# Kernel optimization log

Hardware: AMD Instinct MI355X
Metric: run time of the kernel (lower is better)

## Reference

```python
import jax, jax.numpy as jnp
import numpy as np

D = 64        # symbol_repr_size
NCLS = 10     # n_classes; embedding row NCLS is the 'inf' token
BSZ = 1024
L = 1024      # power of 2 -> perfect segment tree, tree_len = 2*L - 1


def _rms(t):
    # matches: x / x.pow(2).mean(-1,keepdim=True).add(1e-6).sqrt().add(1e-6)
    return t / (jnp.sqrt(jnp.mean(t * t, axis=-1, keepdims=True) + 1e-6) + 1e-6)


def _gate_combine(left, right, Wr):
    # left,right: [b,n,d]; Wr: [2,d,d] (rule weight reshaped).
    # rule(vec(outer(left,right))) == einsum without materializing [b,n,d,d].
    scores = jnp.einsum('bni,kij,bnj->bnk', left, Wr, right)
    alpha = jax.nn.softmax(scores, axis=-1)                      # [b,n,2]
    return _rms(alpha[..., 0:1] * left + alpha[..., 1:2] * right)


def setup_inputs() -> dict:
    key = jax.random.key(0)
    k = jax.random.split(key, 6)
    x = jax.random.randint(k[0], (BSZ, L), 0, NCLS, dtype=jnp.int32)
    a = jax.random.randint(k[1], (BSZ,), 0, L, dtype=jnp.int32)
    b = jax.random.randint(k[2], (BSZ,), 0, L, dtype=jnp.int32)
    return {
        'x': x,
        'query_low': jnp.minimum(a, b),
        'query_high': jnp.maximum(a, b),
        'embedding': jax.random.normal(k[3], (NCLS + 1, D), jnp.float32),
        'rule_w': jax.random.normal(k[4], (2, D * D), jnp.float32) / D,
        'linear_w': jax.random.normal(k[5], (NCLS, D), jnp.float32) / 8.0,
    }


def reference(x, query_low, query_high, embedding, rule_w, linear_w):
    bsz, l = x.shape
    d = embedding.shape[1]
    Wr = rule_w.reshape(2, d, d)
    inf_tok = embedding[-1]                 # [d], the 'inf' token (row n_classes)

    h = _rms(embedding[x])                  # [b,l,d] leaf symbols

    # ---- build neural segment tree, bottom-up (vectorized per level) ----
    levels = [h]                            # levels[0] = leaves (2^depth nodes)
    cur = h
    while cur.shape[1] > 1:
        cur = _gate_combine(cur[:, 0::2], cur[:, 1::2], Wr)
        levels.append(cur)                  # parents of previous level

    # ---- range min query, bottom-up over all nodes (masked per batch) ----
    res = None
    for nodes in levels:                    # leaves first, root last
        n = nodes.shape[1]
        seg = l // n                        # segment length covered per node
        lows = jnp.arange(n, dtype=query_low.dtype) * seg
        highs = lows + (seg - 1)
        inside = (query_low[:, None] <= lows) & (query_high[:, None] >= highs)
        disjoint = (query_low[:, None] > highs) | (query_high[:, None] < lows)
        if res is None:
            # leaf: either fully inside the query range or disjoint from it
            res = jnp.where(inside[..., None], nodes, inf_tok)
        else:
            comb = _gate_combine(res[:, 0::2], res[:, 1::2], Wr)
            res = jnp.where(inside[..., None], nodes,
                            jnp.where(disjoint[..., None], inf_tok, comb))
    returns = res[:, 0]                     # root answer, [b,d]
    return returns @ linear_w.T             # logits [b, n_classes]
```

## Files before the change

kernel.cpp:

```cpp
#include <hip/hip_runtime.h>

#define NCLS 10

typedef _Float16 half8 __attribute__((ext_vector_type(8)));
typedef _Float16 h2 __attribute__((ext_vector_type(2)));
typedef __fp16 fp16x2 __attribute__((ext_vector_type(2)));
typedef float f32x4 __attribute__((ext_vector_type(4)));
typedef unsigned int u32;

#define MFMA(A, B, C) __builtin_amdgcn_mfma_f32_16x16x32_f16(A, B, C, 0, 0, 0)

union U4H8 { uint4 u; half8 h; h2 p[4]; u32 w[4]; };
union U2H4 { uint2 u; h2 p[2]; };
union HCVT { fp16x2 f; h2 h; u32 w; };

__device__ __forceinline__ int rc(int row, int c) { return (row << 3) | (c ^ (row & 7)); }
__device__ __forceinline__ h2 pk2(float a, float b) { HCVT u; u.f = __builtin_amdgcn_cvt_pkrtz(a, b); return u.h; }
__device__ __forceinline__ u32 packh2(float a, float b) { HCVT u; u.f = __builtin_amdgcn_cvt_pkrtz(a, b); return u.w; }
__device__ __forceinline__ float fdot2f(h2 a, h2 b, float c) { return __builtin_amdgcn_fdot2(a, b, c, false); }
__device__ __forceinline__ float wave_sum(float v) {
#pragma unroll
    for (int m = 1; m < 64; m <<= 1) v += __shfl_xor(v, m, 64);
    return v;
}
__device__ __forceinline__ float red4(float v) {
    v += __shfl_xor(v, 16, 64);
    v += __shfl_xor(v, 32, 64);
    return v;
}

template <int N, bool EXACT>
__device__ __forceinline__ void combine(const uint4* src, const int (&rowL)[N],
                                        const int (&rowR)[N], const half8 (&wfd)[2][4],
                                        int pl, int g, U4H8 (&q)[N][2]) {
    U4H8 La[N][2], Ra[N][2];
#pragma unroll
    for (int n = 0; n < N; ++n)
#pragma unroll
        for (int kb = 0; kb < 2; ++kb) {
            La[n][kb].u = src[rc(rowL[n], g + 4 * kb)];
            Ra[n][kb].u = src[rc(rowR[n], g + 4 * kb)];
        }
    const uint2* s2 = (const uint2*)src;
    U2H4 rv[N][4];
#pragma unroll
    for (int n = 0; n < N; ++n)
#pragma unroll
        for (int mb = 0; mb < 4; ++mb)
            rv[n][mb].u = s2[rc(rowR[n], 2 * mb + (g >> 1)) * 2 + (g & 1)];
    float sd[N], lr[N], ll[N], rr[N];
#pragma unroll
    for (int n = 0; n < N; ++n) { sd[n] = 0.f; lr[n] = 0.f; ll[n] = 0.f; rr[n] = 0.f; }
#pragma unroll
    for (int mb = 0; mb < 4; ++mb)
#pragma unroll
        for (int n = 0; n < N; ++n) {
            f32x4 t = {0.f, 0.f, 0.f, 0.f};
#pragma unroll
            for (int kb = 0; kb < 2; ++kb) t = MFMA(wfd[kb][mb], La[n][kb].h, t);
            sd[n] = fdot2f(pk2(t[0], t[1]), rv[n][mb].p[0],
                           fdot2f(pk2(t[2], t[3]), rv[n][mb].p[1], sd[n]));
        }
#pragma unroll
    for (int n = 0; n < N; ++n)
#pragma unroll
        for (int kb = 0; kb < 2; ++kb)
#pragma unroll
            for (int i = 0; i < 4; ++i) {
                h2 l2 = La[n][kb].p[i], r2 = Ra[n][kb].p[i];
                lr[n] = fdot2f(l2, r2, lr[n]);
                if (EXACT) { ll[n] = fdot2f(l2, l2, ll[n]); rr[n] = fdot2f(r2, r2, rr[n]); }
            }
#pragma unroll
    for (int n = 0; n < N; ++n) {
        sd[n] = red4(sd[n]); lr[n] = red4(lr[n]);
        if (EXACT) { ll[n] = red4(ll[n]); rr[n] = red4(rr[n]); }
    }
#pragma unroll
    for (int n = 0; n < N; ++n) {
        float u = __expf(sd[n]);
        float a0 = __builtin_amdgcn_rcpf(1.f + u), a1 = 1.f - a0;
        float ms = EXACT ? (a0 * a0 * ll[n] + 2.f * a0 * a1 * lr[n] + a1 * a1 * rr[n]) * (1.f / 64.f)
                         : a0 * a0 + a1 * a1 + a0 * a1 * lr[n] * (2.f / 64.f);
        float sc = __builtin_amdgcn_rcpf(__builtin_amdgcn_sqrtf(ms + 1e-6f) + 1e-6f);
        h2 c0 = pk2(a0 * sc, a0 * sc), c1 = pk2(a1 * sc, a1 * sc);
#pragma unroll
        for (int kb = 0; kb < 2; ++kb)
#pragma unroll
            for (int i = 0; i < 4; ++i)
                q[n][kb].p[i] = c0 * La[n][kb].p[i] + c1 * Ra[n][kb].p[i];
    }
}


__device__ __forceinline__ void load_wfd(const uint4* ws4, half8 (&wfd)[2][4], int lane) {
#pragma unroll
    for (int fm = 0; fm < 8; ++fm) {
        U4H8 t;
        t.u = ws4[fm * 64 + lane];
        wfd[fm >> 2][fm & 3] = t.h;
    }
}

__global__ void setup_kernel(const float* __restrict__ emb,
                             const float* __restrict__ rule_w, uint4* __restrict__ ws4) {
    int tid = threadIdx.x;
    int idx = blockIdx.x * 256 + tid;
    {
        int e2 = idx & 3, lane = (idx >> 2) & 63, fm = idx >> 8;
        int kb = fm >> 2, mb = fm & 3, pl = lane & 15, g = lane >> 4;
        int i0 = 32 * kb + 8 * g + 2 * e2, j = 16 * mb + pl;
        float d0 = rule_w[4096 + i0 * 64 + j] - rule_w[i0 * 64 + j];
        float d1 = rule_w[4096 + (i0 + 1) * 64 + j] - rule_w[(i0 + 1) * 64 + j];
        ((u32*)ws4)[idx] = packh2(d0, d1);
    }
    if (blockIdx.x == 0 && tid < 64) {
        int lane = tid;
        u32* eg = (u32*)(ws4 + 512);
        for (int r = 0; r < 11; ++r) {
            float e = emb[r * 64 + lane];
            float ms = wave_sum(e * e) * (1.f / 64.f);
            float v = e * __builtin_amdgcn_rcpf(__builtin_amdgcn_sqrtf(ms + 1e-6f) + 1e-6f);
            u32 w = packh2(v, __shfl_xor(v, 1, 64));
            if ((lane & 1) == 0) eg[r * 32 + (lane >> 1)] = w;
        }
        float e = emb[640 + lane];
        u32 w = packh2(e, __shfl_xor(e, 1, 64));
        if ((lane & 1) == 0) eg[11 * 32 + (lane >> 1)] = w;
    }
}

__device__ __forceinline__ void capg(uint4* ws4, long bb, int lev, int node, int lo,
                                     int hi, const U4H8 (&qq)[2], int g) {
    int il = lo >> lev, ih = hi >> lev;
    long base = bb + (long)(128 + lev * 4) * 8;
    if (node == il)       { ws4[base + g] = qq[0].u;      ws4[base + 4 + g] = qq[1].u; }
    if (node == (il ^ 1)) { ws4[base + 8 + g] = qq[0].u;  ws4[base + 12 + g] = qq[1].u; }
    if (node == ih)       { ws4[base + 16 + g] = qq[0].u; ws4[base + 20 + g] = qq[1].u; }
    if (node == (ih ^ 1)) { ws4[base + 24 + g] = qq[0].u; ws4[base + 28 + g] = qq[1].u; }
}

__global__ void __launch_bounds__(256, 3) fold_kernel(
    const int* __restrict__ x, const int* __restrict__ qlo_p,
    const int* __restrict__ qhi_p, uint4* __restrict__ ws4) {
    __shared__ uint4 trs[4 * 64 * 8 + 12 * 8];
    uint4* ermsh = &trs[2048];
    const int tid = threadIdx.x, lane = tid & 63, wid = tid >> 6;
    const int pl = lane & 15, g = lane >> 4;
    const int b = blockIdx.x >> 1, half = blockIdx.x & 1, s = half * 4 + wid;
    const int lo = qlo_p[b], hi = qhi_p[b];

    half8 wfd[2][4];
    load_wfd(ws4, wfd, lane);
    if (tid < 96) { int r = tid >> 3, c = tid & 7; ermsh[rc(r, c)] = ws4[512 + tid]; }
    __syncthreads();

    long bb = 1024 + (long)b * 140 * 8;
    if (half == 0 && wid == 0 && lane < 32) {
        int slot = lane >> 3, c = lane & 7;
        int t = (slot == 0) ? lo : (slot == 1) ? (lo ^ 1) : (slot == 2) ? hi : (hi ^ 1);
        int cls = x[b * 1024 + t];
        ws4[bb + (long)(128 + slot) * 8 + c] = ermsh[rc(cls, c)];
    }

    uint4* wtr = &trs[wid * 512];
    const int2* x2 = (const int2*)x;
    int2 c00 = x2[b * 512 + s * 64 + pl];
    int2 c01 = x2[b * 512 + s * 64 + 16 + pl];
    int2 c10 = x2[b * 512 + s * 64 + 32 + pl];
    int2 c11 = x2[b * 512 + s * 64 + 48 + pl];
    U4H8 q[2][2];
    {
        int rL[2] = {c00.x, c01.x}, rR[2] = {c00.y, c01.y};
        combine<2, false>(ermsh, rL, rR, wfd, pl, g, q);
        wtr[rc(pl, g)] = q[0][0].u;      wtr[rc(pl, g + 4)] = q[0][1].u;
        wtr[rc(16 + pl, g)] = q[1][0].u; wtr[rc(16 + pl, g + 4)] = q[1][1].u;
        capg(ws4, bb, 1, s * 64 + pl, lo, hi, q[0], g);
        capg(ws4, bb, 1, s * 64 + 16 + pl, lo, hi, q[1], g);
    }
    {
        int rL[2] = {c10.x, c11.x}, rR[2] = {c10.y, c11.y};
        combine<2, false>(ermsh, rL, rR, wfd, pl, g, q);
        wtr[rc(32 + pl, g)] = q[0][0].u; wtr[rc(32 + pl, g + 4)] = q[0][1].u;
        wtr[rc(48 + pl, g)] = q[1][0].u; wtr[rc(48 + pl, g + 4)] = q[1][1].u;
        capg(ws4, bb, 1, s * 64 + 32 + pl, lo, hi, q[0], g);
        capg(ws4, bb, 1, s * 64 + 48 + pl, lo, hi, q[1], g);
    }
    {
        int rL[2] = {2 * pl, 32 + 2 * pl}, rR[2] = {2 * pl + 1, 33 + 2 * pl};
        combine<2, false>(wtr, rL, rR, wfd, pl, g, q);
        wtr[rc(pl, g)] = q[0][0].u;      wtr[rc(pl, g + 4)] = q[0][1].u;
        wtr[rc(16 + pl, g)] = q[1][0].u; wtr[rc(16 + pl, g + 4)] = q[1][1].u;
        capg(ws4, bb, 2, s * 32 + pl, lo, hi, q[0], g);
        capg(ws4, bb, 2, s * 32 + 16 + pl, lo, hi, q[1], g);
    }
    {
        int rL[1] = {2 * pl}, rR[1] = {2 * pl + 1};
        U4H8 q1[1][2];
        combine<1, false>(wtr, rL, rR, wfd, pl, g, q1);
        long gr = bb + (long)(s * 16 + pl) * 8;
        ws4[gr + g] = q1[0][0].u;
        ws4[gr + 4 + g] = q1[0][1].u;
    }
}

__global__ void __launch_bounds__(128, 2) topwalk_kernel(
    const int* __restrict__ qlo_p, const int* __restrict__ qhi_p,
    const float* __restrict__ lin_w, float* __restrict__ out,
    uint4* __restrict__ ws4) {
    __shared__ uint4 scr_all[2 * 176 * 8];
    const int tid = threadIdx.x, lane = tid & 63, wid = tid >> 6;
    const int pl = lane & 15, g = lane >> 4;
    const int b = blockIdx.x * 2 + wid;
    const int lo = qlo_p[b], hi = qhi_p[b];

    half8 wfd[2][4];
    load_wfd(ws4, wfd, lane);
    uint4* scr = &scr_all[wid * 176 * 8];
    long bb = 1024 + (long)b * 140 * 8;
    for (int idx = lane; idx < 140 * 8; idx += 64) {
        int r = idx >> 3, c = idx & 7;
        scr[rc(r, c)] = ws4[bb + idx];
    }
    if (lane < 8) scr[rc(172, lane)] = ws4[512 + 88 + lane];
    if (lane < 32) {
        int slot = lane >> 3, c = lane & 7;
        int il3 = lo >> 3, ih3 = hi >> 3;
        int t = (slot == 0) ? il3 : (slot == 1) ? (il3 ^ 1) : (slot == 2) ? ih3 : (ih3 ^ 1);
        scr[rc(140 + slot, c)] = scr[rc(t, c)];
    }

    auto capl = [&](int lev, int node, const U4H8 (&qq)[2]) {
        int il = lo >> lev, ih = hi >> lev, cnt = 1024 >> lev;
        int svb = 128 + lev * 4;
        if (node == il) { scr[rc(svb, g)] = qq[0].u; scr[rc(svb, g + 4)] = qq[1].u; }
        if (((il ^ 1) < cnt) && node == (il ^ 1)) { scr[rc(svb + 1, g)] = qq[0].u; scr[rc(svb + 1, g + 4)] = qq[1].u; }
        if (node == ih) { scr[rc(svb + 2, g)] = qq[0].u; scr[rc(svb + 2, g + 4)] = qq[1].u; }
        if (((ih ^ 1) < cnt) && node == (ih ^ 1)) { scr[rc(svb + 3, g)] = qq[0].u; scr[rc(svb + 3, g + 4)] = qq[1].u; }
    };

    U4H8 q[2][2];
    {
        int rL[2] = {2 * pl, 32 + 2 * pl}, rR[2] = {2 * pl + 1, 33 + 2 * pl};
        combine<2, false>(scr, rL, rR, wfd, pl, g, q);
        scr[rc(pl, g)] = q[0][0].u;      scr[rc(pl, g + 4)] = q[0][1].u;
        scr[rc(16 + pl, g)] = q[1][0].u; scr[rc(16 + pl, g + 4)] = q[1][1].u;
        capl(4, pl, q[0]); capl(4, 16 + pl, q[1]);
    }
    {
        int rL[2] = {64 + 2 * pl, 96 + 2 * pl}, rR[2] = {65 + 2 * pl, 97 + 2 * pl};
        combine<2, false>(scr, rL, rR, wfd, pl, g, q);
        scr[rc(32 + pl, g)] = q[0][0].u; scr[rc(32 + pl, g + 4)] = q[0][1].u;
        scr[rc(48 + pl, g)] = q[1][0].u; scr[rc(48 + pl, g + 4)] = q[1][1].u;
        capl(4, 32 + pl, q[0]); capl(4, 48 + pl, q[1]);
    }
    {
        int rL[2] = {2 * pl, 32 + 2 * pl}, rR[2] = {2 * pl + 1, 33 + 2 * pl};
        combine<2, false>(scr, rL, rR, wfd, pl, g, q);
        scr[rc(pl, g)] = q[0][0].u;      scr[rc(pl, g + 4)] = q[0][1].u;
        scr[rc(16 + pl, g)] = q[1][0].u; scr[rc(16 + pl, g + 4)] = q[1][1].u;
        capl(5, pl, q[0]); capl(5, 16 + pl, q[1]);
    }
    {
        int rL[1] = {2 * pl}, rR[1] = {2 * pl + 1};
        U4H8 q1[1][2];
        combine<1, false>(scr, rL, rR, wfd, pl, g, q1);
        scr[rc(pl, g)] = q1[0][0].u; scr[rc(pl, g + 4)] = q1[0][1].u;
        capl(6, pl, q1[0]);
    }
    int cur_lo = 128, cur_hi = 130;
#pragma unroll 1
    for (int wl = 1; wl <= 10; ++wl) {
        int il = lo >> wl, ih = hi >> wl;
        int ilc = lo >> (wl - 1), ihc = hi >> (wl - 1);
        auto child_row = [&](int c) -> int {
            if (c == ilc) return cur_lo;
            if (c == ihc) return cur_hi;
            int clow = c << (wl - 1);
            int chigh = clow + (1 << (wl - 1)) - 1;
            if (lo <= clow && hi >= chigh)
                return 128 + (wl - 1) * 4 + ((c == (ilc ^ 1)) ? 1 : 3);
            return 172;
        };
        int np = (wl <= 4) ? (16 >> wl) : 0;
        int rowL, rowR, dst;
        bool wm, istree;
        if (pl < np)      { rowL = 2 * pl; rowR = 2 * pl + 1; dst = pl; wm = true; istree = true; }
        else if (pl == 14){ rowL = child_row(2 * il); rowR = child_row(2 * il + 1); dst = 173; wm = true; istree = false; }
        else if (pl == 15){ rowL = child_row(2 * ih); rowR = child_row(2 * ih + 1); dst = 174; wm = true; istree = false; }
        else              { rowL = 0; rowR = 1; dst = 175; wm = false; istree = false; }
        int rLa[1] = {rowL}, rRa[1] = {rowR};
        U4H8 q1[1][2];
        combine<1, true>(scr, rLa, rRa, wfd, pl, g, q1);
        if (wm) { scr[rc(dst, g)] = q1[0][0].u; scr[rc(dst, g + 4)] = q1[0][1].u; }
        if (istree) capl(wl + 6, pl, q1[0]);
        int low = il << wl, high = low + (1 << wl) - 1;
        cur_lo = (lo <= low && hi >= high) ? (128 + wl * 4) : 173;
        int low2 = ih << wl, high2 = low2 + (1 << wl) - 1;
        cur_hi = (lo <= low2 && hi >= high2) ? (128 + wl * 4 + 2) : 174;
    }
    float rv = (float)((_Float16*)scr)[rc(cur_lo, lane >> 3) * 8 + (lane & 7)];
#pragma unroll
    for (int c = 0; c < NCLS; ++c) {
        float s = wave_sum(rv * lin_w[c * 64 + lane]);
        if (lane == 0) out[b * NCLS + c] = s;
    }
}

extern "C" void kernel_launch(void* const* d_in, const int* in_sizes, int n_in,
                              void* d_out, int out_size, void* d_ws, size_t ws_size,
                              hipStream_t stream) {
    const int* x = (const int*)d_in[0];
    const int* qlo = (const int*)d_in[1];
    const int* qhi = (const int*)d_in[2];
    const float* emb = (const float*)d_in[3];
    const float* rule_w = (const float*)d_in[4];
    const float* lin_w = (const float*)d_in[5];
    float* out = (float*)d_out;
    uint4* ws4 = (uint4*)d_ws;
    setup_kernel<<<8, 256, 0, stream>>>(emb, rule_w, ws4);
    fold_kernel<<<2048, 256, 0, stream>>>(x, qlo, qhi, ws4);
    topwalk_kernel<<<512, 128, 0, stream>>>(qlo, qhi, lin_w, out, ws4);
}
```

Before: 57.68 us.

## Split fold into single-wave blocks and move boundary-node capture into topwalk

The fold kernel now launches one 64-thread block per 128-leaf segment, with no block barrier and no per-node capture stores to global memory. It writes only the level-3 nodes. The topwalk kernel runs one wave per batch row and rebuilds the leaf and level-1/level-2 boundary nodes that the range walk needs. It gets them by re-reading the tokens and recombining a few leaf pairs in otherwise idle lanes. This removes the capg branching and scattered global writes from the hot fold and replaces __syncthreads with explicit waitcnts. In exchange, topwalk does a little more compute and the workspace layout changes.

```diff
diff --git a/kernel.cpp b/kernel.cpp
--- a/kernel.cpp
+++ b/kernel.cpp
@@ -91,7 +91,6 @@
                 q[n][kb].p[i] = c0 * La[n][kb].p[i] + c1 * Ra[n][kb].p[i];
     }
 }
-
 
 __device__ __forceinline__ void load_wfd(const uint4* ws4, half8 (&wfd)[2][4], int lane) {
 #pragma unroll
@@ -130,105 +129,94 @@
     }
 }
 
-__device__ __forceinline__ void capg(uint4* ws4, long bb, int lev, int node, int lo,
-                                     int hi, const U4H8 (&qq)[2], int g) {
-    int il = lo >> lev, ih = hi >> lev;
-    long base = bb + (long)(128 + lev * 4) * 8;
-    if (node == il)       { ws4[base + g] = qq[0].u;      ws4[base + 4 + g] = qq[1].u; }
-    if (node == (il ^ 1)) { ws4[base + 8 + g] = qq[0].u;  ws4[base + 12 + g] = qq[1].u; }
-    if (node == ih)       { ws4[base + 16 + g] = qq[0].u; ws4[base + 20 + g] = qq[1].u; }
-    if (node == (ih ^ 1)) { ws4[base + 24 + g] = qq[0].u; ws4[base + 28 + g] = qq[1].u; }
-}
-
-__global__ void __launch_bounds__(256, 3) fold_kernel(
-    const int* __restrict__ x, const int* __restrict__ qlo_p,
-    const int* __restrict__ qhi_p, uint4* __restrict__ ws4) {
-    __shared__ uint4 trs[4 * 64 * 8 + 12 * 8];
-    uint4* ermsh = &trs[2048];
-    const int tid = threadIdx.x, lane = tid & 63, wid = tid >> 6;
+__global__ void __launch_bounds__(64, 4) fold_kernel(
+    const int* __restrict__ x, uint4* __restrict__ ws4) {
+    __shared__ uint4 trs[(64 + 12) * 8];
+    const int lane = threadIdx.x;
     const int pl = lane & 15, g = lane >> 4;
-    const int b = blockIdx.x >> 1, half = blockIdx.x & 1, s = half * 4 + wid;
-    const int lo = qlo_p[b], hi = qhi_p[b];
+    const int b = blockIdx.x >> 3, s = blockIdx.x & 7;
 
     half8 wfd[2][4];
     load_wfd(ws4, wfd, lane);
-    if (tid < 96) { int r = tid >> 3, c = tid & 7; ermsh[rc(r, c)] = ws4[512 + tid]; }
-    __syncthreads();
-
-    long bb = 1024 + (long)b * 140 * 8;
-    if (half == 0 && wid == 0 && lane < 32) {
-        int slot = lane >> 3, c = lane & 7;
-        int t = (slot == 0) ? lo : (slot == 1) ? (lo ^ 1) : (slot == 2) ? hi : (hi ^ 1);
-        int cls = x[b * 1024 + t];
-        ws4[bb + (long)(128 + slot) * 8 + c] = ermsh[rc(cls, c)];
-    }
-
-    uint4* wtr = &trs[wid * 512];
+    {
+        int r = lane >> 3, c = lane & 7;
+        trs[rc(64 + r, c)] = ws4[512 + lane];
+        int idx = lane + 64;
+        if (idx < 96) { r = idx >> 3; c = idx & 7; trs[rc(64 + r, c)] = ws4[512 + idx]; }
+    }
     const int2* x2 = (const int2*)x;
     int2 c00 = x2[b * 512 + s * 64 + pl];
     int2 c01 = x2[b * 512 + s * 64 + 16 + pl];
     int2 c10 = x2[b * 512 + s * 64 + 32 + pl];
     int2 c11 = x2[b * 512 + s * 64 + 48 + pl];
+    asm volatile("s_waitcnt lgkmcnt(0) vmcnt(0)" ::: "memory");
+
     U4H8 q[2][2];
     {
-        int rL[2] = {c00.x, c01.x}, rR[2] = {c00.y, c01.y};
-        combine<2, false>(ermsh, rL, rR, wfd, pl, g, q);
-        wtr[rc(pl, g)] = q[0][0].u;      wtr[rc(pl, g + 4)] = q[0][1].u;
-        wtr[rc(16 + pl, g)] = q[1][0].u; wtr[rc(16 + pl, g + 4)] = q[1][1].u;
-        capg(ws4, bb, 1, s * 64 + pl, lo, hi, q[0], g);
-        capg(ws4, bb, 1, s * 64 + 16 + pl, lo, hi, q[1], g);
-    }
-    {
-        int rL[2] = {c10.x, c11.x}, rR[2] = {c10.y, c11.y};
-        combine<2, false>(ermsh, rL, rR, wfd, pl, g, q);
-        wtr[rc(32 + pl, g)] = q[0][0].u; wtr[rc(32 + pl, g + 4)] = q[0][1].u;
-        wtr[rc(48 + pl, g)] = q[1][0].u; wtr[rc(48 + pl, g + 4)] = q[1][1].u;
-        capg(ws4, bb, 1, s * 64 + 32 + pl, lo, hi, q[0], g);
-        capg(ws4, bb, 1, s * 64 + 48 + pl, lo, hi, q[1], g);
-    }
+        int rL[2] = {64 + c00.x, 64 + c01.x}, rR[2] = {64 + c00.y, 64 + c01.y};
+        combine<2, false>(trs, rL, rR, wfd, pl, g, q);
+        trs[rc(pl, g)] = q[0][0].u;      trs[rc(pl, g + 4)] = q[0][1].u;
+        trs[rc(16 + pl, g)] = q[1][0].u; trs[rc(16 + pl, g + 4)] = q[1][1].u;
+    }
+    {
+        int rL[2] = {64 + c10.x, 64 + c11.x}, rR[2] = {64 + c10.y, 64 + c11.y};
+        combine<2, false>(trs, rL, rR, wfd, pl, g, q);
+        trs[rc(32 + pl, g)] = q[0][0].u; trs[rc(32 + pl, g + 4)] = q[0][1].u;
+        trs[rc(48 + pl, g)] = q[1][0].u; trs[rc(48 + pl, g + 4)] = q[1][1].u;
+    }
+    asm volatile("s_waitcnt lgkmcnt(0)" ::: "memory");
     {
         int rL[2] = {2 * pl, 32 + 2 * pl}, rR[2] = {2 * pl + 1, 33 + 2 * pl};
-        combine<2, false>(wtr, rL, rR, wfd, pl, g, q);
-        wtr[rc(pl, g)] = q[0][0].u;      wtr[rc(pl, g + 4)] = q[0][1].u;
-        wtr[rc(16 + pl, g)] = q[1][0].u; wtr[rc(16 + pl, g + 4)] = q[1][1].u;
-        capg(ws4, bb, 2, s * 32 + pl, lo, hi, q[0], g);
-        capg(ws4, bb, 2, s * 32 + 16 + pl, lo, hi, q[1], g);
-    }
+        combine<2, false>(trs, rL, rR, wfd, pl, g, q);
+        trs[rc(pl, g)] = q[0][0].u;      trs[rc(pl, g + 4)] = q[0][1].u;
+        trs[rc(16 + pl, g)] = q[1][0].u; trs[rc(16 + pl, g + 4)] = q[1][1].u;
+    }
+    asm volatile("s_waitcnt lgkmcnt(0)" ::: "memory");
     {
         int rL[1] = {2 * pl}, rR[1] = {2 * pl + 1};
         U4H8 q1[1][2];
-        combine<1, false>(wtr, rL, rR, wfd, pl, g, q1);
-        long gr = bb + (long)(s * 16 + pl) * 8;
+        combine<1, false>(trs, rL, rR, wfd, pl, g, q1);
+        long gr = 1024 + (long)(b * 128 + s * 16 + pl) * 8;
         ws4[gr + g] = q1[0][0].u;
         ws4[gr + 4 + g] = q1[0][1].u;
     }
 }
 
-__global__ void __launch_bounds__(128, 2) topwalk_kernel(
-    const int* __restrict__ qlo_p, const int* __restrict__ qhi_p,
-    const float* __restrict__ lin_w, float* __restrict__ out,
-    uint4* __restrict__ ws4) {
-    __shared__ uint4 scr_all[2 * 176 * 8];
-    const int tid = threadIdx.x, lane = tid & 63, wid = tid >> 6;
+__global__ void __launch_bounds__(64, 2) topwalk_kernel(
+    const int* __restrict__ x, const int* __restrict__ qlo_p,
+    const int* __restrict__ qhi_p, const float* __restrict__ lin_w,
+    float* __restrict__ out, const uint4* __restrict__ ws4) {
+    __shared__ uint4 scr[196 * 8];
+    const int lane = threadIdx.x;
     const int pl = lane & 15, g = lane >> 4;
-    const int b = blockIdx.x * 2 + wid;
+    const int b = blockIdx.x;
     const int lo = qlo_p[b], hi = qhi_p[b];
 
     half8 wfd[2][4];
     load_wfd(ws4, wfd, lane);
-    uint4* scr = &scr_all[wid * 176 * 8];
-    long bb = 1024 + (long)b * 140 * 8;
-    for (int idx = lane; idx < 140 * 8; idx += 64) {
+    {
+        int r = lane >> 3, c = lane & 7;
+        scr[rc(184 + r, c)] = ws4[512 + lane];
+        int idx = lane + 64;
+        if (idx < 96) { r = idx >> 3; c = idx & 7; scr[rc(184 + r, c)] = ws4[512 + idx]; }
+    }
+#pragma unroll
+    for (int i = 0; i < 16; ++i) {
+        int idx = i * 64 + lane;
         int r = idx >> 3, c = idx & 7;
-        scr[rc(r, c)] = ws4[bb + idx];
-    }
-    if (lane < 8) scr[rc(172, lane)] = ws4[512 + 88 + lane];
+        scr[rc(r, c)] = ws4[1024 + (long)b * 1024 + idx];
+    }
+    asm volatile("s_waitcnt lgkmcnt(0) vmcnt(0)" ::: "memory");
     if (lane < 32) {
         int slot = lane >> 3, c = lane & 7;
         int il3 = lo >> 3, ih3 = hi >> 3;
-        int t = (slot == 0) ? il3 : (slot == 1) ? (il3 ^ 1) : (slot == 2) ? ih3 : (ih3 ^ 1);
-        scr[rc(140 + slot, c)] = scr[rc(t, c)];
-    }
+        int t3 = (slot == 0) ? il3 : (slot == 1) ? (il3 ^ 1) : (slot == 2) ? ih3 : (ih3 ^ 1);
+        scr[rc(140 + slot, c)] = scr[rc(t3, c)];
+        int t0 = (slot == 0) ? lo : (slot == 1) ? (lo ^ 1) : (slot == 2) ? hi : (hi ^ 1);
+        int cls = x[b * 1024 + t0];
+        scr[rc(128 + slot, c)] = scr[rc(184 + cls, c)];
+    }
+    asm volatile("s_waitcnt lgkmcnt(0) vmcnt(0)" ::: "memory");
 
     auto capl = [&](int lev, int node, const U4H8 (&qq)[2]) {
         int il = lo >> lev, ih = hi >> lev, cnt = 1024 >> lev;
@@ -254,6 +242,7 @@
         scr[rc(48 + pl, g)] = q[1][0].u; scr[rc(48 + pl, g + 4)] = q[1][1].u;
         capl(4, 32 + pl, q[0]); capl(4, 48 + pl, q[1]);
     }
+    asm volatile("s_waitcnt lgkmcnt(0)" ::: "memory");
     {
         int rL[2] = {2 * pl, 32 + 2 * pl}, rR[2] = {2 * pl + 1, 33 + 2 * pl};
         combine<2, false>(scr, rL, rR, wfd, pl, g, q);
@@ -261,13 +250,36 @@
         scr[rc(16 + pl, g)] = q[1][0].u; scr[rc(16 + pl, g + 4)] = q[1][1].u;
         capl(5, pl, q[0]); capl(5, 16 + pl, q[1]);
     }
-    {
-        int rL[1] = {2 * pl}, rR[1] = {2 * pl + 1};
-        U4H8 q1[1][2];
-        combine<1, false>(scr, rL, rR, wfd, pl, g, q1);
-        scr[rc(pl, g)] = q1[0][0].u; scr[rc(pl, g + 4)] = q1[0][1].u;
-        capl(6, pl, q1[0]);
-    }
+    asm volatile("s_waitcnt lgkmcnt(0)" ::: "memory");
+    const int il1 = lo >> 1, ih1 = hi >> 1, il2 = lo >> 2, ih2 = hi >> 2;
+    {
+        const int2* x2 = (const int2*)x;
+        bool aact = pl < 8;
+        int n1 = 0;
+        if (aact) {
+            int base2 = (pl < 4) ? ((pl < 2) ? il2 : (il2 ^ 1))
+                                 : ((pl < 6) ? ih2 : (ih2 ^ 1));
+            n1 = 2 * base2 + (pl & 1);
+        }
+        int2 lv = aact ? x2[b * 512 + n1] : make_int2(0, 0);
+        int rL[2] = {2 * pl, aact ? 184 + lv.x : 184};
+        int rR[2] = {2 * pl + 1, aact ? 184 + lv.y : 184};
+        combine<2, false>(scr, rL, rR, wfd, pl, g, q);
+        scr[rc(pl, g)] = q[0][0].u; scr[rc(pl, g + 4)] = q[0][1].u;
+        capl(6, pl, q[0]);
+        if (aact) { scr[rc(175 + pl, g)] = q[1][0].u; scr[rc(175 + pl, g + 4)] = q[1][1].u; }
+    }
+    asm volatile("s_waitcnt lgkmcnt(0)" ::: "memory");
+    if (lane < 32) {
+        int slot = lane >> 3, c = lane & 7;
+        int srcrow = (slot == 0) ? 175 + (il1 & 1)
+                   : (slot == 1) ? 175 + ((il1 & 1) ^ 1)
+                   : (slot == 2) ? 179 + (ih1 & 1)
+                                 : 179 + ((ih1 & 1) ^ 1);
+        scr[rc(132 + slot, c)] = scr[rc(srcrow, c)];
+    }
+    asm volatile("s_waitcnt lgkmcnt(0)" ::: "memory");
+
     int cur_lo = 128, cur_hi = 130;
 #pragma unroll 1
     for (int wl = 1; wl <= 10; ++wl) {
@@ -280,15 +292,18 @@
             int chigh = clow + (1 << (wl - 1)) - 1;
             if (lo <= clow && hi >= chigh)
                 return 128 + (wl - 1) * 4 + ((c == (ilc ^ 1)) ? 1 : 3);
-            return 172;
+            return 195;
         };
         int np = (wl <= 4) ? (16 >> wl) : 0;
         int rowL, rowR, dst;
-        bool wm, istree;
-        if (pl < np)      { rowL = 2 * pl; rowR = 2 * pl + 1; dst = pl; wm = true; istree = true; }
-        else if (pl == 14){ rowL = child_row(2 * il); rowR = child_row(2 * il + 1); dst = 173; wm = true; istree = false; }
-        else if (pl == 15){ rowL = child_row(2 * ih); rowR = child_row(2 * ih + 1); dst = 174; wm = true; istree = false; }
-        else              { rowL = 0; rowR = 1; dst = 175; wm = false; istree = false; }
+        bool wm = true, istree = false;
+        if (pl < np)       { rowL = 2 * pl; rowR = 2 * pl + 1; dst = pl; istree = true; }
+        else if (wl == 1 && pl >= 8 && pl < 12) {
+            int s2 = pl - 8; rowL = 175 + 2 * s2; rowR = 176 + 2 * s2; dst = 136 + s2;
+        }
+        else if (pl == 14) { rowL = child_row(2 * il); rowR = child_row(2 * il + 1); dst = 173; }
+        else if (pl == 15) { rowL = child_row(2 * ih); rowR = child_row(2 * ih + 1); dst = 174; }
+        else               { rowL = 195; rowR = 195; dst = 175; wm = false; }
         int rLa[1] = {rowL}, rRa[1] = {rowR};
         U4H8 q1[1][2];
         combine<1, true>(scr, rLa, rRa, wfd, pl, g, q1);
@@ -298,6 +313,7 @@
         cur_lo = (lo <= low && hi >= high) ? (128 + wl * 4) : 173;
         int low2 = ih << wl, high2 = low2 + (1 << wl) - 1;
         cur_hi = (lo <= low2 && hi >= high2) ? (128 + wl * 4 + 2) : 174;
+        asm volatile("s_waitcnt lgkmcnt(0)" ::: "memory");
     }
     float rv = (float)((_Float16*)scr)[rc(cur_lo, lane >> 3) * 8 + (lane & 7)];
 #pragma unroll
@@ -319,6 +335,6 @@
     float* out = (float*)d_out;
     uint4* ws4 = (uint4*)d_ws;
     setup_kernel<<<8, 256, 0, stream>>>(emb, rule_w, ws4);
-    fold_kernel<<<2048, 256, 0, stream>>>(x, qlo, qhi, ws4);
-    topwalk_kernel<<<512, 128, 0, stream>>>(qlo, qhi, lin_w, out, ws4);
-}
+    fold_kernel<<<8192, 64, 0, stream>>>(x, ws4);
+    topwalk_kernel<<<1024, 64, 0, stream>>>(x, qlo, qhi, lin_w, out, ws4);
+}
```

New measurement: 54.65 us. -5.3%, faster.
